# Optimization experiments

Hardware: AMD Instinct MI355X
Metric: run time of the kernel (lower is better)

Reference implementation:

```python
import jax, jax.numpy as jnp
import numpy as np

RQ_LEVELS = 4  # init_kwargs: rq_levels


def setup_inputs() -> dict:
    key = jax.random.key(0)
    kz, kc = jax.random.split(key)
    z = jax.random.normal(kz, (32768, 512), dtype=jnp.float32)
    cb = jax.random.normal(kc, (1024, 512), dtype=jnp.float32)
    cb = cb / jnp.linalg.norm(cb, axis=1, keepdims=True)  # F.normalize at init
    return {"z": z, "codebook": cb}


def reference(z, codebook):
    # z: [N, D]; codebook: [K, D]
    K = codebook.shape[0]
    cb_sq = jnp.sum(codebook ** 2, axis=1)  # [K]

    def step(carry, _):
        residual, qsum, closs, usage = carry
        # squared L2 distances: ||r||^2 - 2 r.c + ||c||^2  -> [N, K]
        d = jnp.sum(residual ** 2, axis=1, keepdims=True) - 2.0 * (residual @ codebook.T) + cb_sq[None, :]
        idx = jnp.argmin(d, axis=1)            # [N]
        q = codebook[idx]                      # embedding gather [N, D]
        closs = closs + jnp.mean((residual - jax.lax.stop_gradient(q)) ** 2)
        qsum = qsum + q
        residual = residual - q
        usage = usage + jnp.zeros((K,), jnp.float32).at[idx].add(1.0)  # bincount
        return (residual, qsum, closs, usage), idx

    init = (z, jnp.zeros_like(z), jnp.zeros((), z.dtype), jnp.zeros((K,), jnp.float32))
    (_, qsum, closs, usage), idxs = jax.lax.scan(step, init, None, length=RQ_LEVELS)
    discrete_codes = idxs.T                    # [N, rq_levels]
    z_quantized = z + jax.lax.stop_gradient(qsum - z)  # straight-through
    return z_quantized, closs, discrete_codes, usage
```

## Files before the change

### kernel.cpp

```cpp
#include <hip/hip_runtime.h>

#define NROWS  32768
#define KCODES 1024
#define DDIM   512
#define LEVELS 4

#define CLOSS_OFF (NROWS * DDIM)
#define CODES_OFF (CLOSS_OFF + 1)
#define USAGE_OFF (CODES_OFF + NROWS * LEVELS)

typedef __attribute__((ext_vector_type(8))) short bf16x8;
typedef __attribute__((ext_vector_type(4))) float f32x4;
typedef __attribute__((ext_vector_type(8))) unsigned short u16x8;

__device__ __forceinline__ unsigned short bf16_rn(float f) {
  unsigned int u = __float_as_uint(f);
  return (unsigned short)((u + 0x7FFFu + ((u >> 16) & 1u)) >> 16);
}
__device__ __forceinline__ float bf16_f(unsigned short h) {
  return __uint_as_float(((unsigned int)h) << 16);
}
__device__ __forceinline__ void gload16(const void* g, void* l) {
  __builtin_amdgcn_global_load_lds(
      (const __attribute__((address_space(1))) unsigned int*)g,
      (__attribute__((address_space(3))) unsigned int*)l, 16, 0, 0);
}

__global__ __launch_bounds__(256) void prep_kernel(const float* __restrict__ in,
                                                   float* __restrict__ Rout,
                                                   unsigned short* __restrict__ hi,
                                                   unsigned short* __restrict__ lo,
                                                   int nrows) {
  __shared__ float buf[4][DDIM];
  const int wid  = threadIdx.x >> 6;
  const int lane = threadIdx.x & 63;
  const int row  = blockIdx.x * 4 + wid;
  if (row >= nrows) return;
  const float4* src = reinterpret_cast<const float4*>(in + (size_t)row * DDIM);
  float vals[8];
#pragma unroll
  for (int t = 0; t < 2; ++t) {
    const float4 v = src[lane * 2 + t];
    *reinterpret_cast<float4*>(&buf[wid][lane * 8 + t * 4]) = v;
    vals[t * 4 + 0] = v.x; vals[t * 4 + 1] = v.y;
    vals[t * 4 + 2] = v.z; vals[t * 4 + 3] = v.w;
  }
  u16x8 hh, ll;
#pragma unroll
  for (int e = 0; e < 8; ++e) {
    const unsigned short h = bf16_rn(vals[e]);
    hh[e] = h;
    ll[e] = bf16_rn(__fsub_rn(vals[e], bf16_f(h)));
  }
  *reinterpret_cast<u16x8*>(&hi[(size_t)row * DDIM + lane * 8]) = hh;
  *reinterpret_cast<u16x8*>(&lo[(size_t)row * DDIM + lane * 8]) = ll;
  float chain = 0.0f;
  if (lane < 32) {
    const int base = (lane >> 3) * 128 + (lane & 7);
    float a = buf[wid][base];
    chain = __fmul_rn(a, a);
#pragma unroll
    for (int t = 1; t < 16; ++t) {
      a = buf[wid][base + 8 * t];
      chain = __fadd_rn(chain, __fmul_rn(a, a));
    }
  }
  chain = __fadd_rn(chain, __shfl_xor(chain, 1));
  chain = __fadd_rn(chain, __shfl_xor(chain, 2));
  chain = __fadd_rn(chain, __shfl_xor(chain, 4));
  chain = __fadd_rn(chain, __shfl_xor(chain, 8));
  chain = __fadd_rn(chain, __shfl_xor(chain, 16));
  if (lane == 0) Rout[row] = chain;
}

__global__ __launch_bounds__(256) void gemm_topk_kernel(
    const unsigned short* __restrict__ Ahi, const unsigned short* __restrict__ Alo,
    const unsigned short* __restrict__ Bhi, const unsigned short* __restrict__ Blo,
    const float* __restrict__ Rrow, const float* __restrict__ cbsq,
    unsigned int* __restrict__ keys) {
  __shared__ short As[2][128][32];
  __shared__ short Bs[2][128][32];
  __shared__ unsigned int trip[4][64][3];
  const int tid  = threadIdx.x;
  const int lane = tid & 63;
  const int wid  = tid >> 6;
  const int wrow = (wid >> 1) * 64;
  const int wcol = (wid & 1) * 64;
  const int p    = blockIdx.x;
  const int rg   = (p >> 6) * 8 + (p & 7);
  const int cbk  = (p >> 3) & 7;
  const int c = lane & 15, q = lane >> 4;

  f32x4 acc[4][4];
#pragma unroll
  for (int i = 0; i < 4; ++i)
#pragma unroll
    for (int j = 0; j < 4; ++j) acc[i][j] = (f32x4)0.0f;

  auto STAGE = [&](int ks, int buf) {
    const char* Ab = (const char*)((ks < 32) ? Ahi : Alo);
    const char* Bb = (const char*)((ks >= 16 && ks < 32) ? Blo : Bhi);
    const size_t ko = (size_t)(ks & 15) * 64;
#pragma unroll
    for (int i = 0; i < 2; ++i) {
      const int chunk = i * 4 + wid;
      gload16(Ab + (size_t)(rg * 128 + chunk * 16 + (lane >> 2)) * 1024 + ko + (size_t)(lane & 3) * 16,
              &As[buf][chunk * 16][0]);
      gload16(Bb + (size_t)(cbk * 128 + chunk * 16 + (lane >> 2)) * 1024 + ko + (size_t)(lane & 3) * 16,
              &Bs[buf][chunk * 16][0]);
    }
  };

  STAGE(0, 0);
  __syncthreads();
  for (int ks = 0; ks < 48; ++ks) {
    const int cur = ks & 1;
    if (ks + 1 < 48) STAGE(ks + 1, cur ^ 1);
    bf16x8 ar[4], br[4];
#pragma unroll
    for (int i = 0; i < 4; ++i)
      ar[i] = *reinterpret_cast<const bf16x8*>(&As[cur][wrow + i * 16 + c][q * 8]);
#pragma unroll
    for (int j = 0; j < 4; ++j)
      br[j] = *reinterpret_cast<const bf16x8*>(&Bs[cur][wcol + j * 16 + c][q * 8]);
#pragma unroll
    for (int i = 0; i < 4; ++i)
#pragma unroll
      for (int j = 0; j < 4; ++j)
        acc[i][j] = __builtin_amdgcn_mfma_f32_16x16x32_bf16(ar[i], br[j], acc[i][j], 0, 0, 0);
    __syncthreads();
  }

  float cq[4];
#pragma unroll
  for (int j = 0; j < 4; ++j) cq[j] = cbsq[cbk * 128 + wcol + j * 16 + c];

#pragma unroll
  for (int i = 0; i < 4; ++i) {
    const float4 R4 = *reinterpret_cast<const float4*>(&Rrow[rg * 128 + wrow + i * 16 + q * 4]);
#pragma unroll
    for (int jj = 0; jj < 4; ++jj) {
      const int lrow = wrow + i * 16 + q * 4 + jj;
      const float Rv = (jj == 0) ? R4.x : (jj == 1) ? R4.y : (jj == 2) ? R4.z : R4.w;
      unsigned int v[4];
#pragma unroll
      for (int j = 0; j < 4; ++j) {
        float d = __fadd_rn(__fsub_rn(Rv, __fmul_rn(2.0f, acc[i][j][jj])), cq[j]);
        d = fmaxf(d, 0.0f);
        v[j] = (__float_as_uint(d) & 0xFFFFFF80u) | (unsigned int)(wcol + j * 16 + c);
      }
      const unsigned int m01 = min(v[0], v[1]), M01 = max(v[0], v[1]);
      const unsigned int m23 = min(v[2], v[3]), M23 = max(v[2], v[3]);
      unsigned int s0 = min(m01, m23);
      const unsigned int x = max(m01, m23), mM = min(M01, M23);
      unsigned int s1 = min(x, mM);
      unsigned int s2 = min(max(x, mM), max(M01, M23));
#pragma unroll
      for (int m = 1; m < 16; m <<= 1) {
        const unsigned int t0 = (unsigned int)__shfl_xor((int)s0, m);
        const unsigned int t1 = (unsigned int)__shfl_xor((int)s1, m);
        const unsigned int t2 = (unsigned int)__shfl_xor((int)s2, m);
        const unsigned int bb = max(s0, t0), aa = min(s1, t1);
        const unsigned int r0 = min(s0, t0);
        const unsigned int r1 = min(bb, aa);
        const unsigned int r2 = min(max(bb, aa), min(s2, t2));
        s0 = r0; s1 = r1; s2 = r2;
      }
      if (c == 0) {
        trip[wid][lrow & 63][0] = s0;
        trip[wid][lrow & 63][1] = s1;
        trip[wid][lrow & 63][2] = s2;
      }
    }
  }
  __syncthreads();
  if ((wid & 1) == 0) {
    const unsigned int a0 = trip[wid][lane][0], a1 = trip[wid][lane][1], a2 = trip[wid][lane][2];
    const unsigned int b0 = trip[wid + 1][lane][0], b1 = trip[wid + 1][lane][1], b2 = trip[wid + 1][lane][2];
    const unsigned int bb = max(a0, b0), aa = min(a1, b1);
    const unsigned int s0 = min(a0, b0);
    const unsigned int s1 = min(bb, aa);
    const unsigned int s2 = min(max(bb, aa), min(a2, b2));
    const int row = rg * 128 + (wid >> 1) * 64 + lane;
    unsigned int* kp = keys + (size_t)row * 24 + cbk * 3;
    kp[0] = s0; kp[1] = s1; kp[2] = s2;
  }
}

__global__ __launch_bounds__(256) void level_finish_kernel(
    const unsigned int* __restrict__ keys, const float* rin, float* rout,
    const float* __restrict__ cb, const float* __restrict__ cbsq,
    float* __restrict__ Rrow, float* __restrict__ usage,
    float* __restrict__ codes, unsigned short* __restrict__ Ahi,
    unsigned short* __restrict__ Alo, int level, int do_split) {
  __shared__ float buf[4][DDIM];
  const int wid  = threadIdx.x >> 6;
  const int lane = threadIdx.x & 63;
  const int row  = blockIdx.x * 4 + wid;

  const unsigned int k = (lane < 24) ? keys[(size_t)row * 24 + lane] : 0xFFFFFFFFu;
  const int mycode = (lane < 24) ? ((lane / 3) * 128 + (int)(k & 127u)) : 0x7FFFFFFF;
  const float Rv_old = Rrow[row];
  unsigned int g = k;
#pragma unroll
  for (int m = 1; m < 64; m <<= 1) g = min(g, (unsigned int)__shfl_xor((int)g, m));
  const float dmin = __uint_as_float(g & 0xFFFFFF80u);
  const float W = 0.010f + 5.0e-4f * sqrtf(Rv_old);
  const bool cand = (lane < 24) && (__uint_as_float(k & 0xFFFFFF80u) <= dmin + W);
  const unsigned long long mask = __ballot(cand);
  int winner;
  if (__popcll(mask) == 1) {
    int w = cand ? mycode : 0x7FFFFFFF;
#pragma unroll
    for (int m = 1; m < 64; m <<= 1) w = min(w, __shfl_xor(w, m));
    winner = w;
  } else {
    float db = __builtin_inff();
    int   ib = 0x7FFFFFFF;
    if (cand) {
      const float4* rr = reinterpret_cast<const float4*>(rin + (size_t)row * DDIM);
      const float4* cc = reinterpret_cast<const float4*>(cb + (size_t)mycode * DDIM);
      float p = 0.0f;
      for (int t = 0; t < DDIM / 4; ++t) {
        const float4 a = rr[t], b = cc[t];
        p = fmaf(a.x, b.x, p); p = fmaf(a.y, b.y, p);
        p = fmaf(a.z, b.z, p); p = fmaf(a.w, b.w, p);
      }
      db = __fadd_rn(__fsub_rn(Rv_old, __fmul_rn(2.0f, p)), cbsq[mycode]);
      ib = mycode;
    }
#pragma unroll
    for (int m = 1; m < 64; m <<= 1) {
      const float od = __shfl_xor(db, m);
      const int   oi = __shfl_xor(ib, m);
      if (od < db || (od == db && oi < ib)) { db = od; ib = oi; }
    }
    winner = ib;
  }

  const float4* r4 = reinterpret_cast<const float4*>(rin + (size_t)row * DDIM) + lane * 2;
  const float4* q4 = reinterpret_cast<const float4*>(cb + (size_t)winner * DDIM) + lane * 2;
  float4* o4 = reinterpret_cast<float4*>(rout + (size_t)row * DDIM) + lane * 2;
  float vals[8];
#pragma unroll
  for (int t = 0; t < 2; ++t) {
    float4 r = r4[t], qv = q4[t], o;
    o.x = __fsub_rn(r.x, qv.x);
    o.y = __fsub_rn(r.y, qv.y);
    o.z = __fsub_rn(r.z, qv.z);
    o.w = __fsub_rn(r.w, qv.w);
    o4[t] = o;
    *reinterpret_cast<float4*>(&buf[wid][lane * 8 + t * 4]) = o;
    vals[t * 4 + 0] = o.x; vals[t * 4 + 1] = o.y;
    vals[t * 4 + 2] = o.z; vals[t * 4 + 3] = o.w;
  }
  if (do_split) {
    u16x8 hh, ll;
#pragma unroll
    for (int e = 0; e < 8; ++e) {
      const unsigned short h = bf16_rn(vals[e]);
      hh[e] = h;
      ll[e] = bf16_rn(__fsub_rn(vals[e], bf16_f(h)));
    }
    *reinterpret_cast<u16x8*>(&Ahi[(size_t)row * DDIM + lane * 8]) = hh;
    *reinterpret_cast<u16x8*>(&Alo[(size_t)row * DDIM + lane * 8]) = ll;
  }
  float chain = 0.0f;
  if (lane < 32) {
    const int base = (lane >> 3) * 128 + (lane & 7);
    float a = buf[wid][base];
    chain = __fmul_rn(a, a);
#pragma unroll
    for (int t = 1; t < 16; ++t) {
      a = buf[wid][base + 8 * t];
      chain = __fadd_rn(chain, __fmul_rn(a, a));
    }
  }
  chain = __fadd_rn(chain, __shfl_xor(chain, 1));
  chain = __fadd_rn(chain, __shfl_xor(chain, 2));
  chain = __fadd_rn(chain, __shfl_xor(chain, 4));
  chain = __fadd_rn(chain, __shfl_xor(chain, 8));
  chain = __fadd_rn(chain, __shfl_xor(chain, 16));
  if (lane == 0) {
    Rrow[row] = chain;
    atomicAdd(&usage[winner], 1.0f);
    codes[(size_t)row * LEVELS + level] = (float)winner;
  }
}

#define BM 64
#define BN 256
#define DT 32
#define LDP (DT + 4)

__global__ __launch_bounds__(256) void argmin_kernel(const float* __restrict__ res,
                                                     const float* __restrict__ cb,
                                                     const float* __restrict__ Rr_,
                                                     const float* __restrict__ cbsq,
                                                     float* __restrict__ codes,
                                                     int level) {
  __shared__ float As_[BM][LDP];
  __shared__ float Bs_[BN][LDP];
  const int tid = threadIdx.x;
  const int tx = tid & 15;
  const int ty = tid >> 4;
  const size_t brow = (size_t)blockIdx.x * BM;
  float minv[4]; int mini[4]; float Rv[4];
#pragma unroll
  for (int i = 0; i < 4; ++i) { minv[i] = __builtin_inff(); mini[i] = 0; Rv[i] = Rr_[brow + ty + 16 * i]; }
  for (int nc = 0; nc < KCODES; nc += BN) {
    float acc[4][16];
#pragma unroll
    for (int i = 0; i < 4; ++i)
#pragma unroll
      for (int j = 0; j < 16; ++j) acc[i][j] = 0.0f;
    for (int dt = 0; dt < DDIM; dt += DT) {
      __syncthreads();
#pragma unroll
      for (int qq = 0; qq < 2; ++qq) {
        const int ff = tid + qq * 256; const int r = ff >> 3; const int seg = (ff & 7) * 4;
        *reinterpret_cast<float4*>(&As_[r][seg]) =
            *reinterpret_cast<const float4*>(&res[(brow + r) * DDIM + dt + seg]);
      }
#pragma unroll
      for (int qq = 0; qq < 8; ++qq) {
        const int ff = tid + qq * 256; const int r = ff >> 3; const int seg = (ff & 7) * 4;
        *reinterpret_cast<float4*>(&Bs_[r][seg]) =
            *reinterpret_cast<const float4*>(&cb[(size_t)(nc + r) * DDIM + dt + seg]);
      }
      __syncthreads();
#pragma unroll
      for (int dd = 0; dd < DT; dd += 4) {
        float4 av[4];
#pragma unroll
        for (int i = 0; i < 4; ++i) av[i] = *reinterpret_cast<const float4*>(&As_[ty + 16 * i][dd]);
#pragma unroll
        for (int j = 0; j < 16; ++j) {
          const float4 bv = *reinterpret_cast<const float4*>(&Bs_[tx + 16 * j][dd]);
#pragma unroll
          for (int i = 0; i < 4; ++i) {
            acc[i][j] = fmaf(av[i].x, bv.x, acc[i][j]);
            acc[i][j] = fmaf(av[i].y, bv.y, acc[i][j]);
            acc[i][j] = fmaf(av[i].z, bv.z, acc[i][j]);
            acc[i][j] = fmaf(av[i].w, bv.w, acc[i][j]);
          }
        }
      }
    }
#pragma unroll
    for (int j = 0; j < 16; ++j) {
      const int code = nc + tx + 16 * j;
      const float cq = cbsq[code];
#pragma unroll
      for (int i = 0; i < 4; ++i) {
        const float dist = __fadd_rn(__fsub_rn(Rv[i], __fmul_rn(2.0f, acc[i][j])), cq);
        if (dist < minv[i]) { minv[i] = dist; mini[i] = code; }
      }
    }
  }
#pragma unroll
  for (int m = 1; m < 16; m <<= 1) {
#pragma unroll
    for (int i = 0; i < 4; ++i) {
      const float ov = __shfl_xor(minv[i], m);
      const int   oi = __shfl_xor(mini[i], m);
      if (ov < minv[i] || (ov == minv[i] && oi < mini[i])) { minv[i] = ov; mini[i] = oi; }
    }
  }
  if (tx == 0) {
#pragma unroll
    for (int i = 0; i < 4; ++i)
      codes[(brow + ty + 16 * i) * LEVELS + level] = (float)mini[i];
  }
}

__global__ __launch_bounds__(256) void sub_split_rowsq_kernel(
    const float* rin, float* rout, const float* __restrict__ cb,
    const float* __restrict__ codes, float* __restrict__ usage,
    float* __restrict__ Rout, int level) {
  __shared__ float buf[4][DDIM];
  const int wid  = threadIdx.x >> 6;
  const int lane = threadIdx.x & 63;
  const int row  = blockIdx.x * 4 + wid;
  const int idx = (int)codes[(size_t)row * LEVELS + level];
  const float4* r4 = reinterpret_cast<const float4*>(rin + (size_t)row * DDIM) + lane * 2;
  const float4* q4 = reinterpret_cast<const float4*>(cb + (size_t)idx * DDIM) + lane * 2;
  float4* o4 = reinterpret_cast<float4*>(rout + (size_t)row * DDIM) + lane * 2;
#pragma unroll
  for (int t = 0; t < 2; ++t) {
    float4 r = r4[t], q = q4[t], o;
    o.x = __fsub_rn(r.x, q.x);
    o.y = __fsub_rn(r.y, q.y);
    o.z = __fsub_rn(r.z, q.z);
    o.w = __fsub_rn(r.w, q.w);
    o4[t] = o;
    *reinterpret_cast<float4*>(&buf[wid][lane * 8 + t * 4]) = o;
  }
  float chain = 0.0f;
  if (lane < 32) {
    const int base = (lane >> 3) * 128 + (lane & 7);
    float a = buf[wid][base];
    chain = __fmul_rn(a, a);
#pragma unroll
    for (int t = 1; t < 16; ++t) {
      a = buf[wid][base + 8 * t];
      chain = __fadd_rn(chain, __fmul_rn(a, a));
    }
  }
  chain = __fadd_rn(chain, __shfl_xor(chain, 1));
  chain = __fadd_rn(chain, __shfl_xor(chain, 2));
  chain = __fadd_rn(chain, __shfl_xor(chain, 4));
  chain = __fadd_rn(chain, __shfl_xor(chain, 8));
  chain = __fadd_rn(chain, __shfl_xor(chain, 16));
  if (lane == 0) {
    Rout[row] = chain;
    atomicAdd(&usage[idx], 1.0f);
  }
}

__global__ __launch_bounds__(256) void sumR_kernel(const float* __restrict__ R,
                                                   float* __restrict__ slot) {
  const int t = blockIdx.x * 256 + threadIdx.x;
  float s = 0.0f;
#pragma unroll
  for (int k = 0; k < 4; ++k) s += R[t + k * 8192];
#pragma unroll
  for (int m = 1; m < 64; m <<= 1) s += __shfl_xor(s, m);
  __shared__ float ws[4];
  if ((threadIdx.x & 63) == 0) ws[threadIdx.x >> 6] = s;
  __syncthreads();
  if (threadIdx.x == 0) atomicAdd(slot, ((ws[0] + ws[1]) + (ws[2] + ws[3])));
}

__global__ __launch_bounds__(256) void finalize_zq_kernel(const float* __restrict__ z,
                                                          const float* __restrict__ cb,
                                                          const float* __restrict__ codes,
                                                          float* __restrict__ zq) {
  const int row  = (int)((blockIdx.x * 256 + threadIdx.x) >> 6);
  const int lane = threadIdx.x & 63;
  int c[4];
#pragma unroll
  for (int l = 0; l < 4; ++l) c[l] = (int)codes[(size_t)row * LEVELS + l];
#pragma unroll
  for (int t = 0; t < 2; ++t) {
    const int o = lane * 8 + t * 4;
    float4 s = *reinterpret_cast<const float4*>(&cb[(size_t)c[0] * DDIM + o]);
#pragma unroll
    for (int l = 1; l < 4; ++l) {
      const float4 q = *reinterpret_cast<const float4*>(&cb[(size_t)c[l] * DDIM + o]);
      s.x = __fadd_rn(s.x, q.x);
      s.y = __fadd_rn(s.y, q.y);
      s.z = __fadd_rn(s.z, q.z);
      s.w = __fadd_rn(s.w, q.w);
    }
    const float4 zz = *reinterpret_cast<const float4*>(&z[(size_t)row * DDIM + o]);
    float4 r;
    r.x = __fadd_rn(zz.x, __fsub_rn(s.x, zz.x));
    r.y = __fadd_rn(zz.y, __fsub_rn(s.y, zz.y));
    r.z = __fadd_rn(zz.z, __fsub_rn(s.z, zz.z));
    r.w = __fadd_rn(zz.w, __fsub_rn(s.w, zz.w));
    *reinterpret_cast<float4*>(&zq[(size_t)row * DDIM + o]) = r;
  }
}

__global__ void closs_final_kernel(const float* __restrict__ acc, float* __restrict__ out) {
  if (threadIdx.x == 0 && blockIdx.x == 0) {
    float c = 0.0f;
#pragma unroll
    for (int l = 0; l < 4; ++l)
      c = __fadd_rn(c, __fmul_rn(acc[l], 0x1p-24f));
    out[0] = c;
  }
}

extern "C" void kernel_launch(void* const* d_in, const int* in_sizes, int n_in,
                              void* d_out, int out_size, void* d_ws, size_t ws_size,
                              hipStream_t stream) {
  const float* z  = (const float*)d_in[0];
  const float* cb = (const float*)d_in[1];
  float* out   = (float*)d_out;
  float* zq    = out;
  float* closs = out + CLOSS_OFF;
  float* codes = out + CODES_OFF;
  float* usage = out + USAGE_OFF;

  float* R    = (float*)d_ws;
  float* cbsq = R + NROWS;
  float* cacc = cbsq + KCODES;

  const size_t WS_NEED = (size_t)(NROWS + KCODES + 4) * 4
                       + (size_t)NROWS * 24 * 4
                       + 2ull * KCODES * DDIM * 2
                       + 2ull * NROWS * DDIM * 2;

  hipMemsetAsync(usage, 0, KCODES * sizeof(float), stream);
  hipMemsetAsync(cacc, 0, LEVELS * sizeof(float), stream);

  if (ws_size >= WS_NEED) {
    unsigned int*   keys = (unsigned int*)(cacc + 4);
    unsigned short* Bhi  = (unsigned short*)(keys + (size_t)NROWS * 24);
    unsigned short* Blo  = Bhi + (size_t)KCODES * DDIM;
    unsigned short* Ahi  = Blo + (size_t)KCODES * DDIM;
    unsigned short* Alo  = Ahi + (size_t)NROWS * DDIM;

    prep_kernel<<<NROWS / 4, 256, 0, stream>>>(z, R, Ahi, Alo, NROWS);
    prep_kernel<<<KCODES / 4, 256, 0, stream>>>(cb, cbsq, Bhi, Blo, KCODES);

    for (int l = 0; l < LEVELS; ++l) {
      const float* res = (l == 0) ? z : zq;
      gemm_topk_kernel<<<2048, 256, 0, stream>>>(Ahi, Alo, Bhi, Blo, R, cbsq, keys);
      level_finish_kernel<<<NROWS / 4, 256, 0, stream>>>(keys, res, zq, cb, cbsq, R,
                                                         usage, codes, Ahi, Alo, l,
                                                         (l < 3) ? 1 : 0);
      sumR_kernel<<<32, 256, 0, stream>>>(R, cacc + l);
    }
  } else {
    prep_kernel<<<NROWS / 4, 256, 0, stream>>>(z, R, (unsigned short*)(cacc + 4),
                                               (unsigned short*)(cacc + 4) + NROWS, NROWS);
    prep_kernel<<<KCODES / 4, 256, 0, stream>>>(cb, cbsq, (unsigned short*)(cacc + 4),
                                                (unsigned short*)(cacc + 4) + KCODES, KCODES);
    for (int l = 0; l < LEVELS; ++l) {
      const float* res = (l == 0) ? z : zq;
      argmin_kernel<<<NROWS / BM, 256, 0, stream>>>(res, cb, R, cbsq, codes, l);
      sub_split_rowsq_kernel<<<NROWS / 4, 256, 0, stream>>>(res, zq, cb, codes, usage, R, l);
      sumR_kernel<<<32, 256, 0, stream>>>(R, cacc + l);
    }
  }

  finalize_zq_kernel<<<NROWS / 4, 256, 0, stream>>>(z, cb, codes, zq);
  closs_final_kernel<<<1, 64, 0, stream>>>(cacc, closs);
}
```

Baseline: 951.1 us.

## Rework top-k GEMM with 256x128 tiles, triple-buffered LDS ring, swizzled layout

The bf16 hi/lo split arrays are now written with an XOR swizzle on the 16-byte chunk index, so the GEMM can load 64-wide K tiles into LDS without bank conflicts. The GEMM kernel moves to 512-thread blocks covering 256 rows by 128 codes, with a 3-stage LDS ring and prefetch two steps ahead. Explicit vmcnt waits, barriers and setprio are used to overlap global loads with MFMA. This aims to cut per-step synchronisation and LDS conflicts and to reuse each B tile across more rows, at the cost of more LDS per block (about 150KB) and therefore lower occupancy.

Result: faster. 819.5 us (-13.8%).

```diff
diff --git a/kernel.cpp b/kernel.cpp
--- a/kernel.cpp
+++ b/kernel.cpp
@@ -52,8 +52,9 @@
     hh[e] = h;
     ll[e] = bf16_rn(__fsub_rn(vals[e], bf16_f(h)));
   }
-  *reinterpret_cast<u16x8*>(&hi[(size_t)row * DDIM + lane * 8]) = hh;
-  *reinterpret_cast<u16x8*>(&lo[(size_t)row * DDIM + lane * 8]) = ll;
+  const int pos = (lane & 56) | ((lane & 7) ^ (row & 7));
+  *reinterpret_cast<u16x8*>(&hi[(size_t)row * DDIM + pos * 8]) = hh;
+  *reinterpret_cast<u16x8*>(&lo[(size_t)row * DDIM + pos * 8]) = ll;
   float chain = 0.0f;
   if (lane < 32) {
     const int base = (lane >> 3) * 128 + (lane & 7);
@@ -73,81 +74,112 @@
   if (lane == 0) Rout[row] = chain;
 }
 
-__global__ __launch_bounds__(256) void gemm_topk_kernel(
+__global__ __launch_bounds__(512) void gemm_topk_kernel(
     const unsigned short* __restrict__ Ahi, const unsigned short* __restrict__ Alo,
     const unsigned short* __restrict__ Bhi, const unsigned short* __restrict__ Blo,
     const float* __restrict__ Rrow, const float* __restrict__ cbsq,
     unsigned int* __restrict__ keys) {
-  __shared__ short As[2][128][32];
-  __shared__ short Bs[2][128][32];
-  __shared__ unsigned int trip[4][64][3];
+  __shared__ short ring[3][24576];
+  __shared__ unsigned int trip[8][64][3];
   const int tid  = threadIdx.x;
   const int lane = tid & 63;
   const int wid  = tid >> 6;
-  const int wrow = (wid >> 1) * 64;
-  const int wcol = (wid & 1) * 64;
-  const int p    = blockIdx.x;
-  const int rg   = (p >> 6) * 8 + (p & 7);
-  const int cbk  = (p >> 3) & 7;
+  const int wm = wid >> 1, wn = wid & 1;
   const int c = lane & 15, q = lane >> 4;
+  const int p = blockIdx.x;
+  const int rg  = (p >> 6) * 8 + (p & 7);
+  const int cbk = (p >> 3) & 7;
+  const int rowBase = rg * 256;
+  const int colBase = cbk * 128;
+
+  float4 R4[4];
+  float cq[4];
+#pragma unroll
+  for (int rf = 0; rf < 4; ++rf)
+    R4[rf] = *reinterpret_cast<const float4*>(&Rrow[rowBase + wm * 64 + rf * 16 + q * 4]);
+#pragma unroll
+  for (int cf = 0; cf < 4; ++cf)
+    cq[cf] = cbsq[colBase + wn * 64 + cf * 16 + c];
 
   f32x4 acc[4][4];
 #pragma unroll
-  for (int i = 0; i < 4; ++i)
-#pragma unroll
-    for (int j = 0; j < 4; ++j) acc[i][j] = (f32x4)0.0f;
-
-  auto STAGE = [&](int ks, int buf) {
-    const char* Ab = (const char*)((ks < 32) ? Ahi : Alo);
-    const char* Bb = (const char*)((ks >= 16 && ks < 32) ? Blo : Bhi);
-    const size_t ko = (size_t)(ks & 15) * 64;
-#pragma unroll
-    for (int i = 0; i < 2; ++i) {
-      const int chunk = i * 4 + wid;
-      gload16(Ab + (size_t)(rg * 128 + chunk * 16 + (lane >> 2)) * 1024 + ko + (size_t)(lane & 3) * 16,
-              &As[buf][chunk * 16][0]);
-      gload16(Bb + (size_t)(cbk * 128 + chunk * 16 + (lane >> 2)) * 1024 + ko + (size_t)(lane & 3) * 16,
-              &Bs[buf][chunk * 16][0]);
-    }
+  for (int rf = 0; rf < 4; ++rf)
+#pragma unroll
+    for (int cf = 0; cf < 4; ++cf) acc[rf][cf] = (f32x4)0.0f;
+
+  const char* const Asrc[3] = {(const char*)Ahi, (const char*)Ahi, (const char*)Alo};
+  const char* const Bsrc[3] = {(const char*)Bhi, (const char*)Blo, (const char*)Bhi};
+  const int laneOff = (lane >> 3) * 1024 + (lane & 7) * 16;
+
+  auto STAGE_A = [&](int t, int l) {
+    const int g = wid + 8 * l;
+    const char* src = Asrc[t >> 3] + (size_t)(rowBase + g * 8) * 1024 + (t & 7) * 128 + laneOff;
+    gload16(src, &ring[t % 3][g * 512]);
   };
-
-  STAGE(0, 0);
-  __syncthreads();
-  for (int ks = 0; ks < 48; ++ks) {
-    const int cur = ks & 1;
-    if (ks + 1 < 48) STAGE(ks + 1, cur ^ 1);
-    bf16x8 ar[4], br[4];
-#pragma unroll
-    for (int i = 0; i < 4; ++i)
-      ar[i] = *reinterpret_cast<const bf16x8*>(&As[cur][wrow + i * 16 + c][q * 8]);
-#pragma unroll
-    for (int j = 0; j < 4; ++j)
-      br[j] = *reinterpret_cast<const bf16x8*>(&Bs[cur][wcol + j * 16 + c][q * 8]);
-#pragma unroll
-    for (int i = 0; i < 4; ++i)
-#pragma unroll
-      for (int j = 0; j < 4; ++j)
-        acc[i][j] = __builtin_amdgcn_mfma_f32_16x16x32_bf16(ar[i], br[j], acc[i][j], 0, 0, 0);
-    __syncthreads();
-  }
-
-  float cq[4];
-#pragma unroll
-  for (int j = 0; j < 4; ++j) cq[j] = cbsq[cbk * 128 + wcol + j * 16 + c];
-
-#pragma unroll
-  for (int i = 0; i < 4; ++i) {
-    const float4 R4 = *reinterpret_cast<const float4*>(&Rrow[rg * 128 + wrow + i * 16 + q * 4]);
+  auto STAGE_B = [&](int t, int l) {
+    const int g = wid + 8 * l;
+    const char* src = Bsrc[t >> 3] + (size_t)(colBase + g * 8) * 1024 + (t & 7) * 128 + laneOff;
+    gload16(src, &ring[t % 3][16384 + g * 512]);
+  };
+
+#pragma unroll
+  for (int l = 0; l < 4; ++l) STAGE_A(0, l);
+#pragma unroll
+  for (int l = 0; l < 2; ++l) STAGE_B(0, l);
+#pragma unroll
+  for (int l = 0; l < 4; ++l) STAGE_A(1, l);
+#pragma unroll
+  for (int l = 0; l < 2; ++l) STAGE_B(1, l);
+  asm volatile("s_waitcnt vmcnt(6)" ::: "memory");
+  __builtin_amdgcn_s_barrier();
+  __builtin_amdgcn_sched_barrier(0);
+
+  for (int t = 0; t < 24; ++t) {
+    const short* As = &ring[t % 3][0];
+    const short* Bs = &ring[t % 3][16384];
+#pragma unroll
+    for (int kh = 0; kh < 2; ++kh) {
+      const int ch = ((kh * 4 + q) ^ (c & 7)) * 8;
+      bf16x8 ar[4], br[4];
+#pragma unroll
+      for (int rf = 0; rf < 4; ++rf)
+        ar[rf] = *reinterpret_cast<const bf16x8*>(&As[(wm * 64 + rf * 16 + c) * 64 + ch]);
+#pragma unroll
+      for (int cf = 0; cf < 4; ++cf)
+        br[cf] = *reinterpret_cast<const bf16x8*>(&Bs[(wn * 64 + cf * 16 + c) * 64 + ch]);
+      if (t + 2 < 24) {
+        if (kh == 0) { STAGE_A(t + 2, 0); STAGE_A(t + 2, 1); STAGE_B(t + 2, 0); }
+        else         { STAGE_A(t + 2, 2); STAGE_A(t + 2, 3); STAGE_B(t + 2, 1); }
+      }
+      __builtin_amdgcn_s_barrier();
+      __builtin_amdgcn_sched_barrier(0);
+      __builtin_amdgcn_s_setprio(1);
+#pragma unroll
+      for (int rf = 0; rf < 4; ++rf)
+#pragma unroll
+        for (int cf = 0; cf < 4; ++cf)
+          acc[rf][cf] = __builtin_amdgcn_mfma_f32_16x16x32_bf16(ar[rf], br[cf], acc[rf][cf], 0, 0, 0);
+      __builtin_amdgcn_s_setprio(0);
+      if (kh == 1) {
+        if (t == 22)      asm volatile("s_waitcnt vmcnt(0)" ::: "memory");
+        else if (t < 22)  asm volatile("s_waitcnt vmcnt(6)" ::: "memory");
+      }
+      __builtin_amdgcn_s_barrier();
+      __builtin_amdgcn_sched_barrier(0);
+    }
+  }
+
+#pragma unroll
+  for (int rf = 0; rf < 4; ++rf) {
 #pragma unroll
     for (int jj = 0; jj < 4; ++jj) {
-      const int lrow = wrow + i * 16 + q * 4 + jj;
-      const float Rv = (jj == 0) ? R4.x : (jj == 1) ? R4.y : (jj == 2) ? R4.z : R4.w;
+      const float Rv = (jj == 0) ? R4[rf].x : (jj == 1) ? R4[rf].y : (jj == 2) ? R4[rf].z : R4[rf].w;
       unsigned int v[4];
 #pragma unroll
-      for (int j = 0; j < 4; ++j) {
-        float d = __fadd_rn(__fsub_rn(Rv, __fmul_rn(2.0f, acc[i][j][jj])), cq[j]);
+      for (int cf = 0; cf < 4; ++cf) {
+        float d = __fadd_rn(__fsub_rn(Rv, __fmul_rn(2.0f, acc[rf][cf][jj])), cq[cf]);
         d = fmaxf(d, 0.0f);
-        v[j] = (__float_as_uint(d) & 0xFFFFFF80u) | (unsigned int)(wcol + j * 16 + c);
+        v[cf] = (__float_as_uint(d) & 0xFFFFFF80u) | (unsigned int)(wn * 64 + cf * 16 + c);
       }
       const unsigned int m01 = min(v[0], v[1]), M01 = max(v[0], v[1]);
       const unsigned int m23 = min(v[2], v[3]), M23 = max(v[2], v[3]);
@@ -167,9 +199,10 @@
         s0 = r0; s1 = r1; s2 = r2;
       }
       if (c == 0) {
-        trip[wid][lrow & 63][0] = s0;
-        trip[wid][lrow & 63][1] = s1;
-        trip[wid][lrow & 63][2] = s2;
+        const int lrow = rf * 16 + q * 4 + jj;
+        trip[wid][lrow][0] = s0;
+        trip[wid][lrow][1] = s1;
+        trip[wid][lrow][2] = s2;
       }
     }
   }
@@ -181,7 +214,7 @@
     const unsigned int s0 = min(a0, b0);
     const unsigned int s1 = min(bb, aa);
     const unsigned int s2 = min(max(bb, aa), min(a2, b2));
-    const int row = rg * 128 + (wid >> 1) * 64 + lane;
+    const int row = rowBase + wm * 64 + lane;
     unsigned int* kp = keys + (size_t)row * 24 + cbk * 3;
     kp[0] = s0; kp[1] = s1; kp[2] = s2;
   }
@@ -220,13 +253,13 @@
     if (cand) {
       const float4* rr = reinterpret_cast<const float4*>(rin + (size_t)row * DDIM);
       const float4* cc = reinterpret_cast<const float4*>(cb + (size_t)mycode * DDIM);
-      float p = 0.0f;
+      float pp = 0.0f;
       for (int t = 0; t < DDIM / 4; ++t) {
         const float4 a = rr[t], b = cc[t];
-        p = fmaf(a.x, b.x, p); p = fmaf(a.y, b.y, p);
-        p = fmaf(a.z, b.z, p); p = fmaf(a.w, b.w, p);
-      }
-      db = __fadd_rn(__fsub_rn(Rv_old, __fmul_rn(2.0f, p)), cbsq[mycode]);
+        pp = fmaf(a.x, b.x, pp); pp = fmaf(a.y, b.y, pp);
+        pp = fmaf(a.z, b.z, pp); pp = fmaf(a.w, b.w, pp);
+      }
+      db = __fadd_rn(__fsub_rn(Rv_old, __fmul_rn(2.0f, pp)), cbsq[mycode]);
       ib = mycode;
     }
 #pragma unroll
@@ -262,8 +295,9 @@
       hh[e] = h;
       ll[e] = bf16_rn(__fsub_rn(vals[e], bf16_f(h)));
     }
-    *reinterpret_cast<u16x8*>(&Ahi[(size_t)row * DDIM + lane * 8]) = hh;
-    *reinterpret_cast<u16x8*>(&Alo[(size_t)row * DDIM + lane * 8]) = ll;
+    const int pos = (lane & 56) | ((lane & 7) ^ (row & 7));
+    *reinterpret_cast<u16x8*>(&Ahi[(size_t)row * DDIM + pos * 8]) = hh;
+    *reinterpret_cast<u16x8*>(&Alo[(size_t)row * DDIM + pos * 8]) = ll;
   }
   float chain = 0.0f;
   if (lane < 32) {
@@ -508,7 +542,7 @@
 
     for (int l = 0; l < LEVELS; ++l) {
       const float* res = (l == 0) ? z : zq;
-      gemm_topk_kernel<<<2048, 256, 0, stream>>>(Ahi, Alo, Bhi, Blo, R, cbsq, keys);
+      gemm_topk_kernel<<<1024, 512, 0, stream>>>(Ahi, Alo, Bhi, Blo, R, cbsq, keys);
       level_finish_kernel<<<NROWS / 4, 256, 0, stream>>>(keys, res, zq, cb, cbsq, R,
                                                          usage, codes, Ahi, Alo, l,
                                                          (l < 3) ? 1 : 0);
```
